# Kernel optimization log

Measured on AMD Instinct MI355X. Metric: run time of the kernel, lower is better.

## Reference

```python
import jax, jax.numpy as jnp
import numpy as np

B, N, C = 4, 2304, 256
H = 8                      # num_heads
D = C // H                 # head_dim = 32
SCALE = D ** -0.5
H_DS, W_DS = 48, 48
UP = 2                     # spatial_down_ratio
EPS = 1e-5


def setup_inputs() -> dict:
    key = jax.random.key(0)
    ks = jax.random.split(key, 16)
    g = lambda k, shape, s: (jax.random.normal(k, shape, dtype=jnp.float32) * s)
    return {
        "x1": g(ks[0], (B, N, C), 1.0),
        "x2": g(ks[1], (B, N, C), 1.0),
        # attention projections (torch Linear convention: [out, in], no bias)
        "q1_w": g(ks[2], (C, C), C ** -0.5),
        "kv1_w": g(ks[3], (2 * C, C), C ** -0.5),
        "q2_w": g(ks[4], (C, C), C ** -0.5),
        "kv2_w": g(ks[5], (2 * C, C), C ** -0.5),
        # per-head scalar biases
        "beta12": jnp.full((H,), 0.2, dtype=jnp.float32),
        "beta21": jnp.full((H,), 0.1, dtype=jnp.float32),
        # output projections
        "p1_w": g(ks[6], (C, C), (2.0 / C) ** 0.5),
        "p1_b": g(ks[7], (C,), 1e-2),
        "p2_w": g(ks[8], (C, C), (2.0 / C) ** 0.5),
        "p2_b": g(ks[9], (C,), 1e-2),
        # LayerNorm affine params
        "g1": jnp.ones((C,), dtype=jnp.float32),
        "b1": jnp.zeros((C,), dtype=jnp.float32),
        "g2": jnp.ones((C,), dtype=jnp.float32),
        "b2": jnp.zeros((C,), dtype=jnp.float32),
    }


def _heads(x):
    # [B,N,C] -> [B,H,N,D]
    return x.reshape(B, N, H, D).transpose(0, 2, 1, 3)


def _merge(x):
    # [B,H,N,D] -> [B,N,C]
    return x.transpose(0, 2, 1, 3).reshape(B, N, C)


def _cross_attn(q, k, v, beta):
    # scores: [B,H,N,N] with per-head scalar bias
    s = jnp.einsum("bhqd,bhkd->bhqk", q, k) * SCALE + beta[None, :, None, None]
    a = jax.nn.softmax(s, axis=-1)
    return jnp.einsum("bhqk,bhkd->bhqd", a, v)


def _layernorm(x, g, b):
    mu = jnp.mean(x, axis=-1, keepdims=True)
    var = jnp.var(x, axis=-1, keepdims=True)
    return (x - mu) * jax.lax.rsqrt(var + EPS) * g + b


def _forward(x1, x2, q1_w, kv1_w, q2_w, kv2_w, beta12, beta21,
             p1_w, p1_b, p2_w, p2_b, g1, b1, g2, b2):
    q1 = _heads(x1 @ q1_w.T)
    kv1 = x1 @ kv1_w.T          # [B,N,2C]
    k1, v1 = _heads(kv1[..., :C]), _heads(kv1[..., C:])
    q2 = _heads(x2 @ q2_w.T)
    kv2 = x2 @ kv2_w.T
    k2, v2 = _heads(kv2[..., :C]), _heads(kv2[..., C:])

    o1 = _merge(_cross_attn(q1, k2, v2, beta12))   # x1 attends to x2
    o2 = _merge(_cross_attn(q2, k1, v1, beta21))   # x2 attends to x1

    y1 = _layernorm(jax.nn.relu(o1 @ p1_w.T + p1_b), g1, b1)
    y2 = _layernorm(jax.nn.relu(o2 @ p2_w.T + p2_b), g2, b2)

    # [B,N,C] -> [B,C,H_ds,W_ds]
    y1 = y1.transpose(0, 2, 1).reshape(B, C, H_DS, W_DS)
    y2 = y2.transpose(0, 2, 1).reshape(B, C, H_DS, W_DS)

    # bilinear upsample x2, align_corners=False (half-pixel == jax.image default)
    out_shape = (B, C, H_DS * UP, W_DS * UP)
    y1 = jax.image.resize(y1, out_shape, method="bilinear")
    y2 = jax.image.resize(y2, out_shape, method="bilinear")
    return y1, y2


def reference(x1, x2, q1_w, kv1_w, q2_w, kv2_w, beta12, beta21,
              p1_w, p1_b, p2_w, p2_b, g1, b1, g2, b2):
    return _forward(x1, x2, q1_w, kv1_w, q2_w, kv2_w, beta12, beta21,
                    p1_w, p1_b, p2_w, p2_b, g1, b1, g2, b2)
```

## Files before the change

kernel.cpp:

```cpp
#include <hip/hip_runtime.h>
#include <math.h>


typedef __attribute__((ext_vector_type(8))) short short8;
typedef __attribute__((ext_vector_type(4))) float f32x4;
typedef __attribute__((ext_vector_type(16))) float f32x16;
typedef __attribute__((ext_vector_type(2))) unsigned uint32x2;

#define MFMA16(a, b, c) __builtin_amdgcn_mfma_f32_16x16x32_bf16((a), (b), (c), 0, 0, 0)
#define MFMA32(a, b, c) __builtin_amdgcn_mfma_f32_32x32x16_bf16((a), (b), (c), 0, 0, 0)

__device__ __forceinline__ float bf2f(ushort u) {
    union { unsigned u; float f; } x; x.u = ((unsigned)u) << 16; return x.f;
}
__device__ __forceinline__ ushort f2bf(float f) {
    union { float f; unsigned u; } x; x.f = f;
    unsigned u = x.u;
    return (ushort)((u + 0x7fffu + ((u >> 16) & 1u)) >> 16);
}
__device__ __forceinline__ unsigned cvt_pk_bf16(float a, float b) {
    unsigned r;
    asm("v_cvt_pk_bf16_f32 %0, %1, %2" : "=v"(r) : "v"(a), "v"(b));
    return r;
}
__device__ __forceinline__ void plswap(unsigned &a, unsigned &b) {
    uint32x2 r = __builtin_amdgcn_permlane32_swap(a, b, false, false);
    a = r[0]; b = r[1];
}

__global__ void sniff_kernel(const ushort* __restrict__ x, int* __restrict__ flag)
{
    int lane = threadIdx.x;
    ushort u = x[lane * 2];
    int e = (u >> 7) & 0xFF;
    int outlier = (e < 100 || e > 135) ? 1 : 0;
    unsigned long long m = __ballot(outlier);
    if (lane == 0) *flag = (__popcll(m) >= 16) ? 1 : 0;
}

__global__ __launch_bounds__(256) void convert_params(
    const void* s0, const void* s1, const void* s2, const void* s3,
    const void* s4, const void* s5, const void* s6, const void* s7,
    const void* s8, const void* s9, const void* s10, const void* s11,
    ushort* __restrict__ dst, const int* __restrict__ flag)
{
    int idx = blockIdx.x * 256 + threadIdx.x;
    if (idx >= 525824) return;
    const void* src; int off;
    if      (idx < 65536)  { src = s0;  off = idx; }
    else if (idx < 196608) { src = s1;  off = idx - 65536; }
    else if (idx < 262144) { src = s2;  off = idx - 196608; }
    else if (idx < 393216) { src = s3;  off = idx - 262144; }
    else if (idx < 458752) { src = s4;  off = idx - 393216; }
    else if (idx < 524288) { src = s5;  off = idx - 458752; }
    else if (idx < 524544) { src = s6;  off = idx - 524288; }
    else if (idx < 524800) { src = s7;  off = idx - 524544; }
    else if (idx < 525056) { src = s8;  off = idx - 524800; }
    else if (idx < 525312) { src = s9;  off = idx - 525056; }
    else if (idx < 525568) { src = s10; off = idx - 525312; }
    else                   { src = s11; off = idx - 525568; }
    ushort v = (*flag) ? f2bf(((const float*)src)[off])
                       : ((const ushort*)src)[off];
    dst[idx] = v;
}

__global__ __launch_bounds__(256) void convert_x(
    const void* __restrict__ x1, const void* __restrict__ x2,
    ushort* __restrict__ o1, ushort* __restrict__ o2,
    const int* __restrict__ flag)
{
    int idx = blockIdx.x * 256 + threadIdx.x;
    int which = idx >= 294912;
    int off = (which ? idx - 294912 : idx) * 8;
    const void* src = which ? x2 : x1;
    ushort* dst = which ? o2 : o1;
    if (*flag) {
        const float* p = (const float*)src + off;
        float4 a = *(const float4*)p;
        float4 c = *(const float4*)(p + 4);
        uint4 u;
        u.x = cvt_pk_bf16(a.x, a.y);
        u.y = cvt_pk_bf16(a.z, a.w);
        u.z = cvt_pk_bf16(c.x, c.y);
        u.w = cvt_pk_bf16(c.z, c.w);
        *(uint4*)(dst + off) = u;
    } else {
        *(uint4*)(dst + off) = *(const uint4*)((const ushort*)src + off);
    }
}

__global__ __launch_bounds__(256) void gemm_bt(
    const void* __restrict__ Ain, const ushort* __restrict__ W,
    ushort* __restrict__ C, const ushort* __restrict__ bias,
    int M, int N, int K, int relu, const int* __restrict__ dflag, int a_ext,
    int mode, ushort* __restrict__ Kh, ushort* __restrict__ Vt,
    const ushort* __restrict__ W2, const ushort* __restrict__ bias2,
    ushort* __restrict__ Kh2, ushort* __restrict__ Vt2, int mhalf)
{
    __shared__ __align__(16) ushort As[64][40];
    __shared__ __align__(16) ushort Ws[64][40];

    const int m0 = blockIdx.x * 64;
    const int n0 = blockIdx.y * 64;
    const int tid = threadIdx.x;
    const int w = tid >> 6;
    const int lane = tid & 63;
    const int lm = lane & 15;
    const int quad = lane >> 4;
    const int a32 = a_ext ? *dflag : 0;

    const int side = (mhalf && m0 >= mhalf) ? 1 : 0;
    const ushort* Wu = side ? W2 : W;
    const ushort* bu = side ? bias2 : bias;
    ushort* Khu = side ? Kh2 : Kh;
    ushort* Vtu = side ? Vt2 : Vt;

    const f32x4 Z4 = {0.f, 0.f, 0.f, 0.f};
    f32x4 acc[4];
    for (int j = 0; j < 4; j++) acc[j] = Z4;

    const ushort* A16 = (const ushort*)Ain;
    const float*  A32 = (const float*)Ain;
    const int row = tid >> 2, off = (tid & 3) * 8;

    for (int k0 = 0; k0 < K; k0 += 32) {
        __syncthreads();
        if (a32) {
            const float* p0 = A32 + (size_t)(m0 + row) * K + k0 + off;
            float4 f0 = *(const float4*)p0;
            float4 f1 = *(const float4*)(p0 + 4);
            uint4 t0;
            t0.x = cvt_pk_bf16(f0.x, f0.y);
            t0.y = cvt_pk_bf16(f0.z, f0.w);
            t0.z = cvt_pk_bf16(f1.x, f1.y);
            t0.w = cvt_pk_bf16(f1.z, f1.w);
            *(uint4*)&As[row][off] = t0;
        } else {
            *(uint4*)&As[row][off] =
                *(const uint4*)(A16 + (size_t)(m0 + row) * K + k0 + off);
        }
        *(uint4*)&Ws[row][off] =
            *(const uint4*)(Wu + (size_t)(n0 + row) * K + k0 + off);
        __syncthreads();

        short8 af = *(const short8*)&As[w * 16 + lm][quad * 8];
        for (int nt = 0; nt < 4; nt++) {
            short8 wf = *(const short8*)&Ws[nt * 16 + lm][quad * 8];
            acc[nt] = MFMA16(af, wf, acc[nt]);
        }
    }

    const int grow = m0 + w * 16 + quad * 4;
    const int grel = grow - (side ? mhalf : 0);
    if (mode == 1) {
        const float QSC = 0.17677669529663687f * 1.4426950408889634f;
        int bb = grel / 2304;
        int tok = grel - bb * 2304;
        for (int nt = 0; nt < 4; nt++) {
            int col = n0 + nt * 16 + lm;
            if (col < 256) {
                for (int r = 0; r < 4; r++)
                    C[(size_t)(grow + r) * 256 + col] = f2bf(acc[nt][r] * QSC);
            } else if (col < 512) {
                int c2 = col - 256, hh = c2 >> 5, d = c2 & 31;
                for (int r = 0; r < 4; r++)
                    Khu[(((size_t)bb * 8 + hh) * 2304 + tok + r) * 32 + d] = f2bf(acc[nt][r]);
            } else {
                int c2 = col - 512, hh = c2 >> 5, d = c2 & 31;
                uint2 o;
                o.x = cvt_pk_bf16(acc[nt][0], acc[nt][1]);
                o.y = cvt_pk_bf16(acc[nt][2], acc[nt][3]);
                *(uint2*)&Vtu[(((size_t)bb * 8 + hh) * 32 + d) * 2304 + tok] = o;
            }
        }
    } else {
        for (int nt = 0; nt < 4; nt++) {
            int col = n0 + nt * 16 + lm;
            float bv = bu ? bf2f(bu[col]) : 0.f;
            for (int r = 0; r < 4; r++) {
                float v = acc[nt][r] + bv;
                if (relu) v = fmaxf(v, 0.f);
                C[(size_t)(grow + r) * N + col] = f2bf(v);
            }
        }
    }
}

__global__ __launch_bounds__(256) void attn_kernel(
    const ushort* __restrict__ Qa, const ushort* __restrict__ Kha,
    const ushort* __restrict__ Vta, ushort* __restrict__ Oa,
    const ushort* __restrict__ Qb, const ushort* __restrict__ Khb2,
    const ushort* __restrict__ Vtb2, ushort* __restrict__ Ob)
{
    __shared__ __align__(16) ushort Ksh[64][40];
    __shared__ __align__(16) ushort Vsh[32][72];

    const int qb = blockIdx.x;
    const int side = blockIdx.y >> 5;
    const int bh = blockIdx.y & 31;
    const ushort* Q  = side ? Qb   : Qa;
    const ushort* Kh = side ? Khb2 : Kha;
    const ushort* Vt = side ? Vtb2 : Vta;
    ushort* O        = side ? Ob   : Oa;

    const int b = bh >> 3, h = bh & 7;
    const int tid = threadIdx.x;
    const int w = tid >> 6, lane = tid & 63;
    const int l31 = lane & 31, hl = lane >> 5;

    const int qrow = qb * 128 + w * 32 + l31;
    const ushort* qp = Q + ((size_t)b * 2304 + qrow) * 256 + h * 32 + hl * 8;
    short8 qf0 = *(const short8*)qp;
    short8 qf1 = *(const short8*)(qp + 16);

    f32x16 o_acc;
    #pragma unroll
    for (int i = 0; i < 16; i++) o_acc[i] = 0.f;
    const f32x16 Z16 = o_acc;
    float l = 0.f;

    const ushort* Khb = Kh + (size_t)bh * 2304 * 32;
    const ushort* Vtb = Vt + (size_t)bh * 32 * 2304;
    const int ks_row = tid >> 2, ks_off = (tid & 3) * 8;
    const int vs_row = tid >> 3, vs_off = (tid & 7) * 8;

    const ushort* kptr = Khb + (size_t)ks_row * 32 + ks_off;
    const ushort* vptr = Vtb + (size_t)vs_row * 2304 + vs_off;
    uint4 kreg = *(const uint4*)kptr;
    uint4 vreg = *(const uint4*)vptr;

    for (int kc = 0; kc < 36; kc++) {
        __syncthreads();
        *(uint4*)&Ksh[ks_row][ks_off] = kreg;
        *(uint4*)&Vsh[vs_row][vs_off] = vreg;
        __syncthreads();

        int nk = kc < 35 ? kc + 1 : 35;
        kreg = *(const uint4*)(kptr + (size_t)nk * 2048);
        vreg = *(const uint4*)(vptr + nk * 64);

        #pragma unroll
        for (int t = 0; t < 2; t++) {
            short8 kf0 = *(const short8*)&Ksh[t * 32 + l31][hl * 8];
            short8 kf1 = *(const short8*)&Ksh[t * 32 + l31][16 + hl * 8];
            f32x16 s = MFMA32(kf0, qf0, Z16);
            s = MFMA32(kf1, qf1, s);

            float p[16];
            #pragma unroll
            for (int i = 0; i < 16; i++) p[i] = exp2f(s[i]);
            l += (((p[0] + p[1]) + (p[2] + p[3])) + ((p[4] + p[5]) + (p[6] + p[7])))
               + (((p[8] + p[9]) + (p[10] + p[11])) + ((p[12] + p[13]) + (p[14] + p[15])));

            unsigned c0 = cvt_pk_bf16(p[0],  p[1]);
            unsigned c1 = cvt_pk_bf16(p[2],  p[3]);
            unsigned c2 = cvt_pk_bf16(p[4],  p[5]);
            unsigned c3 = cvt_pk_bf16(p[6],  p[7]);
            unsigned c4 = cvt_pk_bf16(p[8],  p[9]);
            unsigned c5 = cvt_pk_bf16(p[10], p[11]);
            unsigned c6 = cvt_pk_bf16(p[12], p[13]);
            unsigned c7 = cvt_pk_bf16(p[14], p[15]);
            plswap(c0, c2);
            plswap(c1, c3);
            plswap(c4, c6);
            plswap(c5, c7);

            union { unsigned u[4]; short8 s8; } pA, pB;
            pA.u[0] = c0; pA.u[1] = c1; pA.u[2] = c2; pA.u[3] = c3;
            pB.u[0] = c4; pB.u[1] = c5; pB.u[2] = c6; pB.u[3] = c7;

            short8 vf0 = *(const short8*)&Vsh[l31][t * 32 + hl * 8];
            short8 vf1 = *(const short8*)&Vsh[l31][t * 32 + 16 + hl * 8];
            o_acc = MFMA32(vf0, pA.s8, o_acc);
            o_acc = MFMA32(vf1, pB.s8, o_acc);
        }
    }

    l += __shfl_xor(l, 32, 64);
    float rl = 1.f / l;
    ushort* op = O + ((size_t)b * 2304 + qrow) * 256 + h * 32 + hl * 4;
    #pragma unroll
    for (int g = 0; g < 4; g++) {
        uint2 o;
        o.x = cvt_pk_bf16(o_acc[4 * g] * rl, o_acc[4 * g + 1] * rl);
        o.y = cvt_pk_bf16(o_acc[4 * g + 2] * rl, o_acc[4 * g + 3] * rl);
        *(uint2*)(op + 8 * g) = o;
    }
}

__global__ __launch_bounds__(256) void lnt_kernel(
    const ushort* __restrict__ Z, const ushort* __restrict__ G1,
    const ushort* __restrict__ B1, const ushort* __restrict__ G2,
    const ushort* __restrict__ B2, ushort* __restrict__ Yt)
{
    __shared__ ushort T[256][72];

    const int tid = threadIdx.x;
    const int tok0 = blockIdx.x * 32;
    const int half = (tok0 >= 9216) ? 1 : 0;
    const int tr = tok0 - half * 9216;
    const int bb = tr / 2304;
    const int tokb = tr - bb * 2304;

    const int tok_l = tid >> 3;
    const int cq = tid & 7;

    const ushort* zp = Z + ((size_t)(tok0 + tok_l)) * 256 + cq * 32;
    uint dd[16];
    for (int i = 0; i < 4; i++) {
        uint4 v = *(const uint4*)(zp + i * 8);
        dd[i * 4 + 0] = v.x; dd[i * 4 + 1] = v.y;
        dd[i * 4 + 2] = v.z; dd[i * 4 + 3] = v.w;
    }
    float s = 0.f, q = 0.f;
    for (int e = 0; e < 16; e++) {
        float x0 = bf2f((ushort)dd[e]);
        float x1 = bf2f((ushort)(dd[e] >> 16));
        s += x0 + x1;
        q += x0 * x0 + x1 * x1;
    }
    s += __shfl_xor(s, 1, 64); q += __shfl_xor(q, 1, 64);
    s += __shfl_xor(s, 2, 64); q += __shfl_xor(q, 2, 64);
    s += __shfl_xor(s, 4, 64); q += __shfl_xor(q, 4, 64);
    float mu = s * (1.f / 256.f);
    float var = q * (1.f / 256.f) - mu * mu;
    float rs = rsqrtf(var + 1e-5f);

    const ushort* Gs = half ? G2 : G1;
    const ushort* Bs = half ? B2 : B1;
    const int col = tok_l + 4 * cq;

    for (int i = 0; i < 4; i++) {
        int cb = cq * 32 + i * 8;
        uint4 gv = *(const uint4*)(Gs + cb);
        uint4 bv = *(const uint4*)(Bs + cb);
        uint gg[4] = {gv.x, gv.y, gv.z, gv.w};
        uint bw[4] = {bv.x, bv.y, bv.z, bv.w};
        for (int k = 0; k < 4; k++) {
            uint u = dd[i * 4 + k];
            float x0 = bf2f((ushort)u), x1 = bf2f((ushort)(u >> 16));
            float y0 = (x0 - mu) * rs * bf2f((ushort)gg[k]) + bf2f((ushort)bw[k]);
            float y1 = (x1 - mu) * rs * bf2f((ushort)(gg[k] >> 16))
                     + bf2f((ushort)(bw[k] >> 16));
            int c = cb + 2 * k;
            T[c][col]     = f2bf(y0);
            T[c + 1][col] = f2bf(y1);
        }
    }
    __syncthreads();

    const int c_row = tid >> 3;
    const int tq = (tid & 7) * 4;
    const size_t obase = ((size_t)((half * 4 + bb) * 256)) * 2304 + tokb + tq;
    for (int i = 0; i < 8; i++) {
        int c = c_row + 32 * i;
        uint2 v = *(const uint2*)&T[c][tq + 4 * i];
        *(uint2*)(Yt + obase + (size_t)c * 2304) = v;
    }
}

__global__ __launch_bounds__(256) void upsample_kernel(
    const ushort* __restrict__ Yt, float* __restrict__ out)
{
    int idx = blockIdx.x * 256 + threadIdx.x;
    int m  = idx % 48;
    int t  = idx / 48;
    int oi = t % 96;
    int bc = t / 96;

    float fi = oi * 0.5f - 0.25f;
    int i0 = (int)floorf(fi);
    float wi = fi - (float)i0;
    int i1 = i0 + 1 < 47 ? i0 + 1 : 47;
    i0 = i0 > 0 ? i0 : 0;
    int jm = m - 1 > 0 ? m - 1 : 0;
    int jp = m + 1 < 47 ? m + 1 : 47;

    const ushort* r0 = Yt + (size_t)bc * 2304 + i0 * 48;
    const ushort* r1 = Yt + (size_t)bc * 2304 + i1 * 48;
    float a0 = bf2f(r0[jm]), b0 = bf2f(r0[m]), c0 = bf2f(r0[jp]);
    float a1 = bf2f(r1[jm]), b1 = bf2f(r1[m]), c1 = bf2f(r1[jp]);
    float u = 1.f - wi;
    float ha = u * a0 + wi * a1;
    float hb = u * b0 + wi * b1;
    float hc = u * c0 + wi * c1;
    float2 o;
    o.x = 0.25f * ha + 0.75f * hb;
    o.y = 0.75f * hb + 0.25f * hc;
    *(float2*)(out + (size_t)bc * 9216 + oi * 96 + m * 2) = o;
}

extern "C" void kernel_launch(void* const* d_in, const int* in_sizes, int n_in,
                              void* d_out, int out_size, void* d_ws, size_t ws_size,
                              hipStream_t stream)
{
    (void)in_sizes; (void)n_in; (void)out_size; (void)ws_size;

    ushort* ws  = (ushort*)d_ws;
    ushort* Q1  = ws;
    ushort* Q2  = Q1  + 2359296;
    ushort* KV1 = Q2  + 2359296;
    ushort* KV2 = KV1 + 4718592;
    ushort* wc  = KV2 + 4718592;
    int*    dflag = (int*)(wc + 525824);

    ushort* cqkv1w = wc;
    ushort* cqkv2w = wc + 196608;
    ushort* cp1w  = wc + 393216;
    ushort* cp2w  = wc + 458752;
    ushort* cp1b  = wc + 524288;
    ushort* cp2b  = wc + 524544;
    ushort* cg1   = wc + 524800;
    ushort* cb1   = wc + 525056;
    ushort* cg2   = wc + 525312;
    ushort* cb2   = wc + 525568;

    float*  outf = (float*)d_out;
    ushort* O1  = (ushort*)d_out;
    ushort* O2  = O1 + 2359296;
    ushort* Xb1 = O2 + 2359296;
    ushort* Xb2 = Xb1 + 2359296;
    ushort* Z1  = KV2;
    ushort* Yt  = Q1;
    (void)Q2; (void)O2; (void)Xb2;

    dim3 blk(256);
    sniff_kernel<<<dim3(1), dim3(64), 0, stream>>>((const ushort*)d_in[0], dflag);
    convert_params<<<dim3(2054), blk, 0, stream>>>(
        d_in[2], d_in[3], d_in[4], d_in[5], d_in[8], d_in[10],
        d_in[9], d_in[11], d_in[12], d_in[13], d_in[14], d_in[15],
        wc, dflag);
    convert_x<<<dim3(2304), blk, 0, stream>>>(d_in[0], d_in[1], Xb1, Xb2, dflag);

    gemm_bt<<<dim3(288, 12), blk, 0, stream>>>(Xb1, cqkv1w, Q1, nullptr,
        18432, 768, 256, 0, dflag, 0, 1, KV1, KV1 + 2359296,
        cqkv2w, nullptr, KV2, KV2 + 2359296, 9216);

    attn_kernel<<<dim3(18, 64), blk, 0, stream>>>(
        Q1, KV2, KV2 + 2359296, O1,
        Q2, KV1, KV1 + 2359296, O2);

    gemm_bt<<<dim3(288, 4), blk, 0, stream>>>(O1, cp1w, Z1, cp1b,
        18432, 256, 256, 1, dflag, 0, 0, nullptr, nullptr,
        cp2w, cp2b, nullptr, nullptr, 9216);

    lnt_kernel<<<dim3(576), blk, 0, stream>>>(Z1, cg1, cb1, cg2, cb2, Yt);

    upsample_kernel<<<dim3(36864), blk, 0, stream>>>(Yt, outf);
}
```

Baseline: 292.1 us.

## Double-buffer K/V tiles in attention with 128-thread blocks and dual accumulators

Restructures the attention kernel to use two-wave 128-thread blocks over 64 query rows, doubling the grid. K/V chunks go into double-buffered shared memory with register prefetch two chunks ahead, so each chunk needs one lightweight barrier instead of two __syncthreads. Two independent output accumulators break the serial MFMA dependency chain and are summed at the end. This adds register pressure, and smaller blocks reload each K/V tile for fewer queries, which raises global/L2 traffic.

```diff
diff --git a/kernel.cpp b/kernel.cpp
--- a/kernel.cpp
+++ b/kernel.cpp
@@ -26,6 +26,10 @@
 __device__ __forceinline__ void plswap(unsigned &a, unsigned &b) {
     uint32x2 r = __builtin_amdgcn_permlane32_swap(a, b, false, false);
     a = r[0]; b = r[1];
+}
+__device__ __forceinline__ void wavebar() {
+    asm volatile("s_waitcnt lgkmcnt(0)" ::: "memory");
+    __builtin_amdgcn_s_barrier();
 }
 
 __global__ void sniff_kernel(const ushort* __restrict__ x, int* __restrict__ flag)
@@ -186,14 +190,14 @@
     }
 }
 
-__global__ __launch_bounds__(256) void attn_kernel(
+__global__ __launch_bounds__(128, 4) void attn_kernel(
     const ushort* __restrict__ Qa, const ushort* __restrict__ Kha,
     const ushort* __restrict__ Vta, ushort* __restrict__ Oa,
     const ushort* __restrict__ Qb, const ushort* __restrict__ Khb2,
     const ushort* __restrict__ Vtb2, ushort* __restrict__ Ob)
 {
-    __shared__ __align__(16) ushort Ksh[64][40];
-    __shared__ __align__(16) ushort Vsh[32][72];
+    __shared__ __align__(16) ushort Ksh[2][64][40];
+    __shared__ __align__(16) ushort Vsh[2][32][72];
 
     const int qb = blockIdx.x;
     const int side = blockIdx.y >> 5;
@@ -208,82 +212,104 @@
     const int w = tid >> 6, lane = tid & 63;
     const int l31 = lane & 31, hl = lane >> 5;
 
-    const int qrow = qb * 128 + w * 32 + l31;
+    const int qrow = qb * 64 + w * 32 + l31;
     const ushort* qp = Q + ((size_t)b * 2304 + qrow) * 256 + h * 32 + hl * 8;
-    short8 qf0 = *(const short8*)qp;
-    short8 qf1 = *(const short8*)(qp + 16);
-
-    f32x16 o_acc;
+    const short8 qf0 = *(const short8*)qp;
+    const short8 qf1 = *(const short8*)(qp + 16);
+
+    f32x16 o0, o1;
     #pragma unroll
-    for (int i = 0; i < 16; i++) o_acc[i] = 0.f;
-    const f32x16 Z16 = o_acc;
+    for (int i = 0; i < 16; i++) { o0[i] = 0.f; o1[i] = 0.f; }
+    const f32x16 Z16 = o0;
     float l = 0.f;
 
     const ushort* Khb = Kh + (size_t)bh * 2304 * 32;
     const ushort* Vtb = Vt + (size_t)bh * 32 * 2304;
-    const int ks_row = tid >> 2, ks_off = (tid & 3) * 8;
-    const int vs_row = tid >> 3, vs_off = (tid & 7) * 8;
-
-    const ushort* kptr = Khb + (size_t)ks_row * 32 + ks_off;
-    const ushort* vptr = Vtb + (size_t)vs_row * 2304 + vs_off;
-    uint4 kreg = *(const uint4*)kptr;
-    uint4 vreg = *(const uint4*)vptr;
-
-    for (int kc = 0; kc < 36; kc++) {
-        __syncthreads();
-        *(uint4*)&Ksh[ks_row][ks_off] = kreg;
-        *(uint4*)&Vsh[vs_row][vs_off] = vreg;
-        __syncthreads();
-
-        int nk = kc < 35 ? kc + 1 : 35;
-        kreg = *(const uint4*)(kptr + (size_t)nk * 2048);
-        vreg = *(const uint4*)(vptr + nk * 64);
-
-        #pragma unroll
-        for (int t = 0; t < 2; t++) {
-            short8 kf0 = *(const short8*)&Ksh[t * 32 + l31][hl * 8];
-            short8 kf1 = *(const short8*)&Ksh[t * 32 + l31][16 + hl * 8];
-            f32x16 s = MFMA32(kf0, qf0, Z16);
-            s = MFMA32(kf1, qf1, s);
-
-            float p[16];
-            #pragma unroll
-            for (int i = 0; i < 16; i++) p[i] = exp2f(s[i]);
-            l += (((p[0] + p[1]) + (p[2] + p[3])) + ((p[4] + p[5]) + (p[6] + p[7])))
-               + (((p[8] + p[9]) + (p[10] + p[11])) + ((p[12] + p[13]) + (p[14] + p[15])));
-
-            unsigned c0 = cvt_pk_bf16(p[0],  p[1]);
-            unsigned c1 = cvt_pk_bf16(p[2],  p[3]);
-            unsigned c2 = cvt_pk_bf16(p[4],  p[5]);
-            unsigned c3 = cvt_pk_bf16(p[6],  p[7]);
-            unsigned c4 = cvt_pk_bf16(p[8],  p[9]);
-            unsigned c5 = cvt_pk_bf16(p[10], p[11]);
-            unsigned c6 = cvt_pk_bf16(p[12], p[13]);
-            unsigned c7 = cvt_pk_bf16(p[14], p[15]);
-            plswap(c0, c2);
-            plswap(c1, c3);
-            plswap(c4, c6);
-            plswap(c5, c7);
-
-            union { unsigned u[4]; short8 s8; } pA, pB;
-            pA.u[0] = c0; pA.u[1] = c1; pA.u[2] = c2; pA.u[3] = c3;
-            pB.u[0] = c4; pB.u[1] = c5; pB.u[2] = c6; pB.u[3] = c7;
-
-            short8 vf0 = *(const short8*)&Vsh[l31][t * 32 + hl * 8];
-            short8 vf1 = *(const short8*)&Vsh[l31][t * 32 + 16 + hl * 8];
-            o_acc = MFMA32(vf0, pA.s8, o_acc);
-            o_acc = MFMA32(vf1, pB.s8, o_acc);
-        }
-    }
+    const int k_r0 = tid >> 2, k_off = (tid & 3) * 8;
+    const int v_r0 = tid >> 3, v_off = (tid & 7) * 8;
+
+#define LOADK(d0, d1, cc) { \
+    const ushort* _kp = Khb + ((size_t)((cc) * 64 + k_r0) * 32) + k_off; \
+    d0 = *(const uint4*)_kp; \
+    d1 = *(const uint4*)(_kp + 32 * 32); \
+}
+#define LOADV(d0, d1, cc) { \
+    const ushort* _vp = Vtb + (size_t)v_r0 * 2304 + (cc) * 64 + v_off; \
+    d0 = *(const uint4*)_vp; \
+    d1 = *(const uint4*)(_vp + 16 * 2304); \
+}
+#define STORE(bi, ka, kb, va, vb) { \
+    *(uint4*)&Ksh[bi][k_r0][k_off]      = ka; \
+    *(uint4*)&Ksh[bi][k_r0 + 32][k_off] = kb; \
+    *(uint4*)&Vsh[bi][v_r0][v_off]      = va; \
+    *(uint4*)&Vsh[bi][v_r0 + 16][v_off] = vb; \
+}
+#define TILE(bi, t, oacc) { \
+    short8 kf0 = *(const short8*)&Ksh[bi][(t) * 32 + l31][hl * 8]; \
+    short8 kf1 = *(const short8*)&Ksh[bi][(t) * 32 + l31][16 + hl * 8]; \
+    f32x16 s = MFMA32(kf0, qf0, Z16); \
+    s = MFMA32(kf1, qf1, s); \
+    float p[16]; \
+    _Pragma("unroll") \
+    for (int i = 0; i < 16; i++) p[i] = exp2f(s[i]); \
+    l += (((p[0] + p[1]) + (p[2] + p[3])) + ((p[4] + p[5]) + (p[6] + p[7]))) \
+       + (((p[8] + p[9]) + (p[10] + p[11])) + ((p[12] + p[13]) + (p[14] + p[15]))); \
+    unsigned c0 = cvt_pk_bf16(p[0],  p[1]); \
+    unsigned c1 = cvt_pk_bf16(p[2],  p[3]); \
+    unsigned c2 = cvt_pk_bf16(p[4],  p[5]); \
+    unsigned c3 = cvt_pk_bf16(p[6],  p[7]); \
+    unsigned c4 = cvt_pk_bf16(p[8],  p[9]); \
+    unsigned c5 = cvt_pk_bf16(p[10], p[11]); \
+    unsigned c6 = cvt_pk_bf16(p[12], p[13]); \
+    unsigned c7 = cvt_pk_bf16(p[14], p[15]); \
+    plswap(c0, c2); plswap(c1, c3); plswap(c4, c6); plswap(c5, c7); \
+    union { unsigned u[4]; short8 s8; } pA, pB; \
+    pA.u[0] = c0; pA.u[1] = c1; pA.u[2] = c2; pA.u[3] = c3; \
+    pB.u[0] = c4; pB.u[1] = c5; pB.u[2] = c6; pB.u[3] = c7; \
+    short8 vf0 = *(const short8*)&Vsh[bi][l31][(t) * 32 + hl * 8]; \
+    short8 vf1 = *(const short8*)&Vsh[bi][l31][(t) * 32 + 16 + hl * 8]; \
+    oacc = MFMA32(vf0, pA.s8, oacc); \
+    oacc = MFMA32(vf1, pB.s8, oacc); \
+}
+
+    uint4 kA0, kA1, vA0, vA1;
+    uint4 kB0, kB1, vB0, vB1;
+
+    LOADK(kA0, kA1, 0); LOADV(vA0, vA1, 0);
+    LOADK(kB0, kB1, 1); LOADV(vB0, vB1, 1);
+    STORE(0, kA0, kA1, vA0, vA1);
+    LOADK(kA0, kA1, 2); LOADV(vA0, vA1, 2);
+    wavebar();
+
+    for (int i = 0; i < 18; i++) {
+        TILE(0, 0, o0); TILE(0, 1, o1);
+        STORE(1, kB0, kB1, vB0, vB1);
+        int c3 = 2 * i + 3; c3 = c3 < 36 ? c3 : 35;
+        LOADK(kB0, kB1, c3); LOADV(vB0, vB1, c3);
+        wavebar();
+        TILE(1, 0, o0); TILE(1, 1, o1);
+        STORE(0, kA0, kA1, vA0, vA1);
+        int c4 = 2 * i + 4; c4 = c4 < 36 ? c4 : 35;
+        LOADK(kA0, kA1, c4); LOADV(vA0, vA1, c4);
+        wavebar();
+    }
+#undef LOADK
+#undef LOADV
+#undef STORE
+#undef TILE
 
     l += __shfl_xor(l, 32, 64);
     float rl = 1.f / l;
     ushort* op = O + ((size_t)b * 2304 + qrow) * 256 + h * 32 + hl * 4;
     #pragma unroll
     for (int g = 0; g < 4; g++) {
+        float e0 = (o0[4 * g]     + o1[4 * g])     * rl;
+        float e1 = (o0[4 * g + 1] + o1[4 * g + 1]) * rl;
+        float e2 = (o0[4 * g + 2] + o1[4 * g + 2]) * rl;
+        float e3 = (o0[4 * g + 3] + o1[4 * g + 3]) * rl;
         uint2 o;
-        o.x = cvt_pk_bf16(o_acc[4 * g] * rl, o_acc[4 * g + 1] * rl);
-        o.y = cvt_pk_bf16(o_acc[4 * g + 2] * rl, o_acc[4 * g + 3] * rl);
+        o.x = cvt_pk_bf16(e0, e1);
+        o.y = cvt_pk_bf16(e2, e3);
         *(uint2*)(op + 8 * g) = o;
     }
 }
@@ -436,7 +462,7 @@
         18432, 768, 256, 0, dflag, 0, 1, KV1, KV1 + 2359296,
         cqkv2w, nullptr, KV2, KV2 + 2359296, 9216);
 
-    attn_kernel<<<dim3(18, 64), blk, 0, stream>>>(
+    attn_kernel<<<dim3(36, 64), dim3(128), 0, stream>>>(
         Q1, KV2, KV2 + 2359296, O1,
         Q2, KV1, KV1 + 2359296, O2);
 
```

After: 467.0 us. 1.6x slower.
